# Optimization experiments

Measured on AMD Instinct MI355X. Metric: run time of the kernel, lower is better.

The kernel has to match this reference:

```python
import jax, jax.numpy as jnp
import numpy as np

LEVELS = np.array([8, 5, 5, 5], dtype=np.int64)
BASIS = np.cumprod(np.concatenate([[1], LEVELS[:-1]])).astype(np.int64)  # [1,8,40,200]
N_E = int(np.prod(LEVELS))  # 1000
BN_EPS = 1e-5
BOUND_EPS = 1e-3


def setup_inputs() -> dict:
    key = jax.random.key(0)
    ks = jax.random.split(key, 3)
    B, C, T, E = 32, 512, 4096, 4
    return {
        "z": jax.random.normal(ks[0], (B, C, T), dtype=jnp.float32),
        "W_in": jax.random.normal(ks[1], (C, E), dtype=jnp.float32) * 0.05,
        "b_in": jnp.zeros((E,), dtype=jnp.float32),
        "gamma": jnp.ones((E,), dtype=jnp.float32),
        "beta": jnp.zeros((E,), dtype=jnp.float32),
        "W_out": jax.random.normal(ks[2], (E, C), dtype=jnp.float32) * 0.05,
        "b_out": jnp.zeros((C,), dtype=jnp.float32),
    }


def _round_ste(x):
    return x + jax.lax.stop_gradient(jnp.round(x) - x)


def reference(z, W_in, b_in, gamma, beta, W_out, b_out):
    levels = jnp.asarray(LEVELS, dtype=jnp.float32)      # [E]
    basis = jnp.asarray(BASIS, dtype=jnp.float32)        # [E]
    half_w = jnp.floor(levels / 2.0)                     # levels // 2
    B, C, T = z.shape
    N = B * T

    # preprocess: 'n c t -> (n t) c'
    x = jnp.transpose(z, (0, 2, 1)).reshape(N, C)        # [N, C]
    # project_in
    h = x @ W_in + b_in                                   # [N, E]
    # BatchNorm1d, training mode (biased batch stats)
    mu = jnp.mean(h, axis=0)
    var = jnp.var(h, axis=0)
    h = (h - mu) * jax.lax.rsqrt(var + BN_EPS) * gamma + beta

    # bound + round_ste quantize
    half_l = (levels - 1.0) * (1.0 - BOUND_EPS) / 2.0
    offset = jnp.where(jnp.mod(levels, 2.0) == 0.0, 0.5, 0.0)
    shift = jnp.tan(offset / half_l)
    bounded = jnp.tanh(h + shift) * half_l - offset
    zhat_n = _round_ste(bounded) / half_w                 # [N, E], normalized codes

    # codes -> indices
    idx = jnp.sum((zhat_n * half_w + half_w) * basis, axis=-1).astype(jnp.int32)  # [N]

    # project_out, '(b t) c -> b c t'
    out = zhat_n @ W_out + b_out                          # [N, C]
    zhat = jnp.transpose(out.reshape(B, T, C), (0, 2, 1))  # [B, C, T]

    commit_loss = jnp.mean((z - jax.lax.stop_gradient(zhat)) ** 2)

    # perplexity via counts (avoids [N, n_e] one-hot)
    counts = jnp.zeros((N_E,), dtype=jnp.float32).at[idx].add(1.0)
    e_mean = counts / N
    perplexity = jnp.exp(-jnp.sum(e_mean * jnp.log(e_mean + 1e-10)))

    return zhat, commit_loss, perplexity
```

## Files before the change

### kernel.cpp

```cpp
#include <hip/hip_runtime.h>
#include <math.h>


namespace {
constexpr int Cv = 512, Tv = 4096, Bv = 32;
constexpr int Nv = Bv * Tv;
constexpr long long TOTv = (long long)Nv * Cv;
constexpr int CSA = 8;
constexpr int NBA = Bv * CSA;

constexpr size_t OFF_HP = 0;
constexpr size_t OFF_GP = OFF_HP + (size_t)NBA * Tv * 16;
constexpr size_t OFF_H  = OFF_GP + (size_t)NBA * Tv * 16;
constexpr size_t OFF_G  = OFF_H  + (size_t)Nv * 16;
constexpr size_t OFF_B1 = OFF_G  + (size_t)Nv * 16;
constexpr size_t OFF_B2 = OFF_B1 + 256 * 2 * 8;
constexpr size_t OFF_CN = OFF_B2 + 512 * 8 * 8;
constexpr size_t OFF_CP = OFF_CN + 32 * 8;
constexpr size_t OFF_CT = OFF_CP + 512 * 8;
constexpr size_t OFF_CD = OFF_CT + 4096;
}

__global__ __launch_bounds__(1024, 4) void fsq_kA(
    const float* __restrict__ z, const float* __restrict__ W_in,
    const float* __restrict__ W_out, const float* __restrict__ b_out,
    float* __restrict__ h_part, float* __restrict__ g_part, double* __restrict__ bs1)
{
    __shared__ float s_wi[64][4];
    __shared__ float s_wo[64][4];
    __shared__ float s_bo[64];
    __shared__ double red[2][1024];

    const int tid = threadIdx.x;
    const int bid = blockIdx.x;
    const int b = bid >> 3;
    const int cs = bid & 7;
    const int c0 = cs << 6;

    if (tid < 64) {
        const int c = c0 + tid;
        *(float4*)&s_wi[tid][0] = *(const float4*)(W_in + c * 4);
        s_wo[tid][0] = W_out[c];
        s_wo[tid][1] = W_out[512 + c];
        s_wo[tid][2] = W_out[1024 + c];
        s_wo[tid][3] = W_out[1536 + c];
        s_bo[tid] = b_out[c];
    }
    __syncthreads();

    float h[4][4] = {}, g[4][4] = {};
    float z2 = 0.f, zb = 0.f;
    const float* zp = z + ((size_t)b * Cv + c0) * Tv + tid * 4;
#pragma unroll 4
    for (int c = 0; c < 64; ++c) {
        const float4 zv = *(const float4*)(zp + (size_t)c * Tv);
        const float4 wi = *(const float4*)&s_wi[c][0];
        const float4 wo = *(const float4*)&s_wo[c][0];
        const float bo = s_bo[c];
        const float zr[4] = {zv.x, zv.y, zv.z, zv.w};
#pragma unroll
        for (int j = 0; j < 4; ++j) {
            h[j][0] = fmaf(zr[j], wi.x, h[j][0]);
            h[j][1] = fmaf(zr[j], wi.y, h[j][1]);
            h[j][2] = fmaf(zr[j], wi.z, h[j][2]);
            h[j][3] = fmaf(zr[j], wi.w, h[j][3]);
            g[j][0] = fmaf(zr[j], wo.x, g[j][0]);
            g[j][1] = fmaf(zr[j], wo.y, g[j][1]);
            g[j][2] = fmaf(zr[j], wo.z, g[j][2]);
            g[j][3] = fmaf(zr[j], wo.w, g[j][3]);
            z2 = fmaf(zr[j], zr[j], z2);
        }
        zb = fmaf((zr[0] + zr[1]) + (zr[2] + zr[3]), bo, zb);
    }

    float* hp = h_part + ((size_t)bid * Tv + tid * 4) * 4;
    float* gp = g_part + ((size_t)bid * Tv + tid * 4) * 4;
#pragma unroll
    for (int j = 0; j < 4; ++j) {
        *(float4*)(hp + j * 4) = make_float4(h[j][0], h[j][1], h[j][2], h[j][3]);
        *(float4*)(gp + j * 4) = make_float4(g[j][0], g[j][1], g[j][2], g[j][3]);
    }

    red[0][tid] = (double)z2;
    red[1][tid] = (double)zb;
    __syncthreads();
    for (int s = 512; s > 0; s >>= 1) {
        if (tid < s) { red[0][tid] += red[0][tid + s]; red[1][tid] += red[1][tid + s]; }
        __syncthreads();
    }
    if (tid == 0) { bs1[bid * 2] = red[0][0]; bs1[bid * 2 + 1] = red[1][0]; }
}

__global__ __launch_bounds__(256) void fsq_kB(
    const float* __restrict__ h_part, const float* __restrict__ g_part,
    const float* __restrict__ b_in,
    float* __restrict__ h_ws, float* __restrict__ g_ws, double* __restrict__ bs2)
{
    __shared__ double red[8][256];
    const int tid = threadIdx.x;
    const int bid = blockIdx.x;
    const int b = bid >> 4;
    const int t = ((bid & 15) << 8) + tid;
    const int n = (b << 12) + t;

    double hd[4];
    hd[0] = (double)b_in[0]; hd[1] = (double)b_in[1];
    hd[2] = (double)b_in[2]; hd[3] = (double)b_in[3];
    float gg[4] = {0.f, 0.f, 0.f, 0.f};
#pragma unroll
    for (int cs = 0; cs < 8; ++cs) {
        const size_t base = ((size_t)(b * 8 + cs) * Tv + t) * 4;
        const float4 p = *(const float4*)(h_part + base);
        const float4 q = *(const float4*)(g_part + base);
        hd[0] += (double)p.x; hd[1] += (double)p.y;
        hd[2] += (double)p.z; hd[3] += (double)p.w;
        gg[0] += q.x; gg[1] += q.y; gg[2] += q.z; gg[3] += q.w;
    }

    *(float4*)(h_ws + (size_t)n * 4) =
        make_float4((float)hd[0], (float)hd[1], (float)hd[2], (float)hd[3]);
    *(float4*)(g_ws + (size_t)n * 4) = make_float4(gg[0], gg[1], gg[2], gg[3]);

#pragma unroll
    for (int e = 0; e < 4; ++e) {
        red[e][tid] = hd[e];
        red[4 + e][tid] = hd[e] * hd[e];
    }
    __syncthreads();
    for (int s = 128; s > 0; s >>= 1) {
        if (tid < s) {
#pragma unroll
            for (int k = 0; k < 8; ++k) red[k][tid] += red[k][tid + s];
        }
        __syncthreads();
    }
    if (tid == 0) {
#pragma unroll
        for (int k = 0; k < 8; ++k) bs2[bid * 8 + k] = red[k][0];
    }
}

__global__ __launch_bounds__(256) void fsq_kS(
    const float* __restrict__ gamma, const float* __restrict__ beta,
    const float* __restrict__ W_out, const float* __restrict__ b_out,
    const double* __restrict__ bs1, const double* __restrict__ bs2,
    double* __restrict__ consts, unsigned* __restrict__ counts)
{
    __shared__ double sbuf[15][256];
    const int tid = threadIdx.x;

    for (int i = tid; i < 1000; i += 256) counts[i] = 0;

    double a[10] = {};
    for (int r = tid; r < 512; r += 256) {
        const double* p = bs2 + (size_t)r * 8;
#pragma unroll
        for (int k = 0; k < 8; ++k) a[k] += p[k];
    }
    a[8] = bs1[tid * 2];
    a[9] = bs1[tid * 2 + 1];
#pragma unroll
    for (int k = 0; k < 10; ++k) sbuf[k][tid] = a[k];
    __syncthreads();
    for (int s = 128; s > 0; s >>= 1) {
        if (tid < s) {
#pragma unroll
            for (int k = 0; k < 10; ++k) sbuf[k][tid] += sbuf[k][tid + s];
        }
        __syncthreads();
    }
    double tot[10];
    if (tid == 0) {
#pragma unroll
        for (int k = 0; k < 10; ++k) tot[k] = sbuf[k][0];
    }
    __syncthreads();

    double gr[15] = {};
    for (int c = tid; c < 512; c += 256) {
        const double w0 = (double)W_out[c], w1 = (double)W_out[512 + c];
        const double w2 = (double)W_out[1024 + c], w3 = (double)W_out[1536 + c];
        const double bb = (double)b_out[c];
        gr[0] += w0 * w0; gr[1] += w0 * w1; gr[2] += w0 * w2; gr[3] += w0 * w3;
        gr[4] += w1 * w1; gr[5] += w1 * w2; gr[6] += w1 * w3;
        gr[7] += w2 * w2; gr[8] += w2 * w3; gr[9] += w3 * w3;
        gr[10] += w0 * bb; gr[11] += w1 * bb; gr[12] += w2 * bb; gr[13] += w3 * bb;
        gr[14] += bb * bb;
    }
#pragma unroll
    for (int k = 0; k < 15; ++k) sbuf[k][tid] = gr[k];
    __syncthreads();
    for (int s = 128; s > 0; s >>= 1) {
        if (tid < s) {
#pragma unroll
            for (int k = 0; k < 15; ++k) sbuf[k][tid] += sbuf[k][tid + s];
        }
        __syncthreads();
    }
    if (tid == 0) {
        const double Ninv = 1.0 / (double)Nv;
#pragma unroll
        for (int e = 0; e < 4; ++e) {
            const double mu = tot[e] * Ninv;
            const double var = tot[4 + e] * Ninv - mu * mu;
            const double sc = (double)gamma[e] / sqrt(var + 1e-5);
            consts[e] = sc;
            consts[4 + e] = (double)beta[e] - mu * sc;
        }
        consts[8] = tot[8];
        consts[9] = tot[9];
#pragma unroll
        for (int k = 0; k < 15; ++k) consts[16 + k] = sbuf[k][0];
        constexpr double hl0 = (8.0 - 1.0) * (1.0 - 1e-3) / 2.0;
        consts[31] = tan(0.5 / hl0);
    }
}

__global__ __launch_bounds__(256) void fsq_kQ(
    const float* __restrict__ h_ws, const float* __restrict__ g_ws,
    const double* __restrict__ consts, unsigned* __restrict__ counts,
    unsigned short* __restrict__ codes, double* __restrict__ cp)
{
    __shared__ double s_cp[4];
    const int tid = threadIdx.x;
    const int lane = tid & 63;
    const int w = tid >> 6;
    const int n = blockIdx.x * 256 + tid;

    const double sc0 = consts[0], sc1 = consts[1], sc2 = consts[2], sc3 = consts[3];
    const double bi0 = consts[4], bi1 = consts[5], bi2 = consts[6], bi3 = consts[7];
    const double shift0 = consts[31];
    constexpr double hl0 = (8.0 - 1.0) * (1.0 - 1e-3) / 2.0;
    constexpr double hl1 = (5.0 - 1.0) * (1.0 - 1e-3) / 2.0;

    const float4 hv = *(const float4*)(h_ws + (size_t)n * 4);
    const double hn0 = fma((double)hv.x, sc0, bi0);
    const double hn1 = fma((double)hv.y, sc1, bi1);
    const double hn2 = fma((double)hv.z, sc2, bi2);
    const double hn3 = fma((double)hv.w, sc3, bi3);
    const double r0 = rint(tanh(hn0 + shift0) * hl0 - 0.5);
    const double r1 = rint(tanh(hn1) * hl1);
    const double r2 = rint(tanh(hn2) * hl1);
    const double r3 = rint(tanh(hn3) * hl1);
    const double zd0 = r0 * 0.25, zd1 = r1 * 0.5, zd2 = r2 * 0.5, zd3 = r3 * 0.5;

    const int code = ((int)r0 + 4) + ((int)r1 + 2) * 8 + ((int)r2 + 2) * 40
                   + ((int)r3 + 2) * 200;
    codes[n] = (unsigned short)code;
    atomicAdd(&counts[code], 1u);

    const float4 gv = *(const float4*)(g_ws + (size_t)n * 4);
    const double cg = zd0 * (double)gv.x + zd1 * (double)gv.y
                    + zd2 * (double)gv.z + zd3 * (double)gv.w;
    double q = consts[16 + 14]
             + 2.0 * (zd0 * consts[16 + 10] + zd1 * consts[16 + 11]
                    + zd2 * consts[16 + 12] + zd3 * consts[16 + 13])
             + zd0 * zd0 * consts[16 + 0] + zd1 * zd1 * consts[16 + 4]
             + zd2 * zd2 * consts[16 + 7] + zd3 * zd3 * consts[16 + 9]
             + 2.0 * (zd0 * zd1 * consts[16 + 1] + zd0 * zd2 * consts[16 + 2]
                    + zd0 * zd3 * consts[16 + 3] + zd1 * zd2 * consts[16 + 5]
                    + zd1 * zd3 * consts[16 + 6] + zd2 * zd3 * consts[16 + 8]);
    double qsum = q - 2.0 * cg;
#pragma unroll
    for (int m = 1; m < 64; m <<= 1) qsum += __shfl_xor(qsum, m, 64);
    if (lane == 0) s_cp[w] = qsum;
    __syncthreads();
    if (tid == 0) cp[blockIdx.x] = (s_cp[0] + s_cp[1]) + (s_cp[2] + s_cp[3]);
}

__global__ __launch_bounds__(256, 2) void fsq_kW(
    const unsigned short* __restrict__ codes, const float* __restrict__ W_out,
    const float* __restrict__ b_out, const double* __restrict__ cp,
    const double* __restrict__ consts, const unsigned* __restrict__ counts,
    float* __restrict__ out, int out_size)
{
    __shared__ float s_p0[4096];
    __shared__ float s_p1[4096];
    __shared__ float s_p2[4096];
    __shared__ float s_p3[4096];
    __shared__ float s_wo[32][4];
    __shared__ float s_bo[32];
    __shared__ double r1[256], r2[256];

    const int tid = threadIdx.x;
    const int bid = blockIdx.x;
    const int b = bid >> 4;
    const int c0 = (bid & 15) << 5;

    if (bid == 0) {
        double c_ = cp[tid] + cp[tid + 256];
        double pl = 0.0;
        for (int i = tid; i < 1000; i += 256) {
            const double em = (double)counts[i] / (double)Nv;
            pl += em * log(em + 1e-10);
        }
        r1[tid] = c_; r2[tid] = pl;
        __syncthreads();
        for (int s = 128; s > 0; s >>= 1) {
            if (tid < s) { r1[tid] += r1[tid + s]; r2[tid] += r2[tid + s]; }
            __syncthreads();
        }
        if (tid == 0) {
            out[out_size - 2] = (float)((consts[8] - 2.0 * consts[9] + r1[0]) / (double)TOTv);
            out[out_size - 1] = (float)exp(-r2[0]);
        }
        __syncthreads();
    }

    if (tid < 32) {
        const int c = c0 + tid;
        s_wo[tid][0] = W_out[c];
        s_wo[tid][1] = W_out[512 + c];
        s_wo[tid][2] = W_out[1024 + c];
        s_wo[tid][3] = W_out[1536 + c];
        s_bo[tid] = b_out[c];
    }
    for (int r = tid; r < 4096; r += 256) {
        const int code = (int)codes[(b << 12) + r];
        const int x0 = code & 7;
        const int c1 = code >> 3;
        const int x1 = c1 % 5;
        const int c2 = c1 / 5;
        const int x2 = c2 % 5;
        const int x3 = c2 / 5;
        s_p0[r] = (float)(x0 - 4) * 0.25f;
        s_p1[r] = (float)(x1 - 2) * 0.5f;
        s_p2[r] = (float)(x2 - 2) * 0.5f;
        s_p3[r] = (float)(x3 - 2) * 0.5f;
    }
    __syncthreads();

    const int w = tid >> 6;
    const int lane = tid & 63;
#pragma unroll
    for (int cc = 0; cc < 8; ++cc) {
        const int ci = w * 8 + cc;
        const float4 wo = *(const float4*)&s_wo[ci][0];
        const float bo = s_bo[ci];
        float* op = out + ((size_t)b * Cv + (c0 + ci)) * Tv;
#pragma unroll 4
        for (int it = 0; it < 64; ++it) {
            const int t = it * 64 + lane;
            const float o = fmaf(s_p0[t], wo.x, fmaf(s_p1[t], wo.y,
                            fmaf(s_p2[t], wo.z, fmaf(s_p3[t], wo.w, bo))));
            op[t] = o;
        }
    }
}

extern "C" void kernel_launch(void* const* d_in, const int* in_sizes, int n_in,
                              void* d_out, int out_size, void* d_ws, size_t ws_size,
                              hipStream_t stream) {
    const float* z     = (const float*)d_in[0];
    const float* W_in  = (const float*)d_in[1];
    const float* b_in  = (const float*)d_in[2];
    const float* gamma = (const float*)d_in[3];
    const float* beta  = (const float*)d_in[4];
    const float* W_out = (const float*)d_in[5];
    const float* b_out = (const float*)d_in[6];
    float* out = (float*)d_out;

    char* ws = (char*)d_ws;
    float*          h_part = (float*)(ws + OFF_HP);
    float*          g_part = (float*)(ws + OFF_GP);
    float*          h_ws   = (float*)(ws + OFF_H);
    float*          g_ws   = (float*)(ws + OFF_G);
    double*         bs1    = (double*)(ws + OFF_B1);
    double*         bs2    = (double*)(ws + OFF_B2);
    double*         consts = (double*)(ws + OFF_CN);
    double*         cp     = (double*)(ws + OFF_CP);
    unsigned*       counts = (unsigned*)(ws + OFF_CT);
    unsigned short* codes  = (unsigned short*)(ws + OFF_CD);

    fsq_kA<<<NBA, 1024, 0, stream>>>(z, W_in, W_out, b_out, h_part, g_part, bs1);
    fsq_kB<<<512, 256, 0, stream>>>(h_part, g_part, b_in, h_ws, g_ws, bs2);
    fsq_kS<<<1, 256, 0, stream>>>(gamma, beta, W_out, b_out, bs1, bs2, consts, counts);
    fsq_kQ<<<512, 256, 0, stream>>>(h_ws, g_ws, consts, counts, codes, cp);
    fsq_kW<<<512, 256, 0, stream>>>(codes, W_out, b_out, cp, consts, counts, out, out_size);
}
```

Measured before the change: 191.8 us.

## Rework output kernel to register-resident codes with vectorized nontemporal stores

The final projection kernel drops its 64 KB of shared-memory code planes. Each of 1024 threads now decodes four consecutive codes into registers and writes float4 rows for 32 channels using nontemporal stores. The partial-sum writes in the first kernel also become nontemporal. The aim is to cut LDS traffic and widen the 256 MB output write stream, at the cost of larger blocks, a changed reduction size in block 0, and possible cache bypass for h_part/g_part, which the next kernel reads back.

```diff
diff --git a/kernel.cpp b/kernel.cpp
--- a/kernel.cpp
+++ b/kernel.cpp
@@ -1,6 +1,8 @@
 #include <hip/hip_runtime.h>
 #include <math.h>
 
+
+typedef float f32x4 __attribute__((ext_vector_type(4)));
 
 namespace {
 constexpr int Cv = 512, Tv = 4096, Bv = 32;
@@ -77,8 +79,10 @@
     float* gp = g_part + ((size_t)bid * Tv + tid * 4) * 4;
 #pragma unroll
     for (int j = 0; j < 4; ++j) {
-        *(float4*)(hp + j * 4) = make_float4(h[j][0], h[j][1], h[j][2], h[j][3]);
-        *(float4*)(gp + j * 4) = make_float4(g[j][0], g[j][1], g[j][2], g[j][3]);
+        f32x4 hv = {h[j][0], h[j][1], h[j][2], h[j][3]};
+        f32x4 gv = {g[j][0], g[j][1], g[j][2], g[j][3]};
+        __builtin_nontemporal_store(hv, (f32x4*)(hp + j * 4));
+        __builtin_nontemporal_store(gv, (f32x4*)(gp + j * 4));
     }
 
     red[0][tid] = (double)z2;
@@ -268,19 +272,15 @@
     if (tid == 0) cp[blockIdx.x] = (s_cp[0] + s_cp[1]) + (s_cp[2] + s_cp[3]);
 }
 
-__global__ __launch_bounds__(256, 2) void fsq_kW(
+__global__ __launch_bounds__(1024, 2) void fsq_kW(
     const unsigned short* __restrict__ codes, const float* __restrict__ W_out,
     const float* __restrict__ b_out, const double* __restrict__ cp,
     const double* __restrict__ consts, const unsigned* __restrict__ counts,
     float* __restrict__ out, int out_size)
 {
-    __shared__ float s_p0[4096];
-    __shared__ float s_p1[4096];
-    __shared__ float s_p2[4096];
-    __shared__ float s_p3[4096];
     __shared__ float s_wo[32][4];
     __shared__ float s_bo[32];
-    __shared__ double r1[256], r2[256];
+    __shared__ double r1[1024], r2[1024];
 
     const int tid = threadIdx.x;
     const int bid = blockIdx.x;
@@ -288,15 +288,15 @@
     const int c0 = (bid & 15) << 5;
 
     if (bid == 0) {
-        double c_ = cp[tid] + cp[tid + 256];
+        double c_ = (tid < 512) ? cp[tid] : 0.0;
         double pl = 0.0;
-        for (int i = tid; i < 1000; i += 256) {
+        for (int i = tid; i < 1000; i += 1024) {
             const double em = (double)counts[i] / (double)Nv;
             pl += em * log(em + 1e-10);
         }
         r1[tid] = c_; r2[tid] = pl;
         __syncthreads();
-        for (int s = 128; s > 0; s >>= 1) {
+        for (int s = 512; s > 0; s >>= 1) {
             if (tid < s) { r1[tid] += r1[tid + s]; r2[tid] += r2[tid + s]; }
             __syncthreads();
         }
@@ -315,36 +315,36 @@
         s_wo[tid][3] = W_out[1536 + c];
         s_bo[tid] = b_out[c];
     }
-    for (int r = tid; r < 4096; r += 256) {
-        const int code = (int)codes[(b << 12) + r];
+    __syncthreads();
+
+    const ushort4 cd = *(const ushort4*)(codes + (b << 12) + tid * 4);
+    float zn[4][4];
+#pragma unroll
+    for (int j = 0; j < 4; ++j) {
+        const int code = (int)((&cd.x)[j]);
         const int x0 = code & 7;
         const int c1 = code >> 3;
         const int x1 = c1 % 5;
         const int c2 = c1 / 5;
         const int x2 = c2 % 5;
         const int x3 = c2 / 5;
-        s_p0[r] = (float)(x0 - 4) * 0.25f;
-        s_p1[r] = (float)(x1 - 2) * 0.5f;
-        s_p2[r] = (float)(x2 - 2) * 0.5f;
-        s_p3[r] = (float)(x3 - 2) * 0.5f;
-    }
-    __syncthreads();
-
-    const int w = tid >> 6;
-    const int lane = tid & 63;
-#pragma unroll
-    for (int cc = 0; cc < 8; ++cc) {
-        const int ci = w * 8 + cc;
+        zn[j][0] = (float)(x0 - 4) * 0.25f;
+        zn[j][1] = (float)(x1 - 2) * 0.5f;
+        zn[j][2] = (float)(x2 - 2) * 0.5f;
+        zn[j][3] = (float)(x3 - 2) * 0.5f;
+    }
+
+    float* op = out + ((size_t)b * Cv + c0) * Tv + tid * 4;
+#pragma unroll 4
+    for (int ci = 0; ci < 32; ++ci) {
         const float4 wo = *(const float4*)&s_wo[ci][0];
         const float bo = s_bo[ci];
-        float* op = out + ((size_t)b * Cv + (c0 + ci)) * Tv;
-#pragma unroll 4
-        for (int it = 0; it < 64; ++it) {
-            const int t = it * 64 + lane;
-            const float o = fmaf(s_p0[t], wo.x, fmaf(s_p1[t], wo.y,
-                            fmaf(s_p2[t], wo.z, fmaf(s_p3[t], wo.w, bo))));
-            op[t] = o;
-        }
+        f32x4 o;
+#pragma unroll
+        for (int j = 0; j < 4; ++j)
+            o[j] = fmaf(zn[j][0], wo.x, fmaf(zn[j][1], wo.y,
+                   fmaf(zn[j][2], wo.z, fmaf(zn[j][3], wo.w, bo))));
+        __builtin_nontemporal_store(o, (f32x4*)(op + (size_t)ci * Tv));
     }
 }
 
@@ -376,5 +376,5 @@
     fsq_kB<<<512, 256, 0, stream>>>(h_part, g_part, b_in, h_ws, g_ws, bs2);
     fsq_kS<<<1, 256, 0, stream>>>(gamma, beta, W_out, b_out, bs1, bs2, consts, counts);
     fsq_kQ<<<512, 256, 0, stream>>>(h_ws, g_ws, consts, counts, codes, cp);
-    fsq_kW<<<512, 256, 0, stream>>>(codes, W_out, b_out, cp, consts, counts, out, out_size);
-}
+    fsq_kW<<<512, 1024, 0, stream>>>(codes, W_out, b_out, cp, consts, counts, out, out_size);
+}
```

Result: no change. 191.4 us (-0.2%).
